# Kernel tuning notes

Measured on AMD Instinct MI355X. Metric: run time of the kernel, lower is better.

## Reference

```python
import jax, jax.numpy as jnp
import numpy as np
from jax import lax

B, N, S, NS, V = 2, 8192, 1024, 32, 8
CF, CIN, COUT, H1, RADIUS = 64, 70, 128, 32, 0.2
BN_EPS = 1e-5


def _bn(x, g, b, axes):
    m = jnp.mean(x, axes, keepdims=True)
    v = jnp.var(x, axes, keepdims=True)
    return (x - m) / jnp.sqrt(v + BN_EPS) * g + b


def _fps(xyz, s):
    # deterministic farthest point sampling, start index 0
    b, n, _ = xyz.shape
    def step(carry, _):
        dmin, last = carry
        p = jnp.take_along_axis(xyz, last[:, None, None], axis=1)[:, 0]  # [B,3]
        d = jnp.sum((xyz - p[:, None, :]) ** 2, -1)
        dmin = jnp.minimum(dmin, d)
        nxt = jnp.argmax(dmin, axis=-1).astype(jnp.int32)
        return (dmin, nxt), last
    init = (jnp.full((b, n), jnp.inf, xyz.dtype), jnp.zeros((b,), jnp.int32))
    _, idx = lax.scan(step, init, None, length=s)
    idx = jnp.transpose(idx)  # [B,S]
    return jnp.take_along_axis(xyz, idx[..., None], axis=1), idx


def _ball_query(new_xyz, xyz, k, radius):
    # first k points (in original order) within radius; -1 padded, like pytorch3d
    b, s, _ = new_xyz.shape
    n = xyz.shape[1]
    d2 = jnp.sum((new_xyz[:, :, None, :] - xyz[:, None, :, :]) ** 2, -1)  # [B,S,N]
    within = d2 < radius * radius
    slot = jnp.cumsum(within.astype(jnp.int32), axis=-1) - 1
    valid = within & (slot < k)
    slot_c = jnp.where(valid, slot, k)  # dump slot k
    bb = jnp.arange(b)[:, None, None]
    ss = jnp.arange(s)[None, :, None]
    upd = jnp.broadcast_to(jnp.arange(n, dtype=jnp.int32), (b, s, n))
    gidx = jnp.full((b, s, k + 1), -1, jnp.int32).at[bb, ss, slot_c].set(upd)[..., :k]
    return gidx


def reference(xyz, f, mc_idx, gumbel_u, W1_0, b1_0, g1_0, be1_0, W1_1, b1_1,
              W2_0, b2_0, g2_0, be2_0, W2_1, b2_1, Wr, br):
    bsz = xyz.shape[0]
    new_xyz, _ = _fps(xyz, S)                              # [B,S,3]
    gidx = _ball_query(new_xyz, xyz, NS, RADIUS)           # [B,S,n]
    mask = gidx < 0
    safe = jnp.where(mask, 0, gidx)
    bb = jnp.arange(bsz)[:, None, None]
    grouped_xyz = jnp.where(mask[..., None], 0.0, xyz[bb, safe])      # [B,S,n,3]
    grouped_feat = jnp.where(mask[..., None], 0.0, f[bb, safe])       # [B,S,n,CF]
    mc = xyz[:, mc_idx, :]                                 # [B,V,3] (same for all S)

    local = grouped_xyz - new_xyz[:, :, None, :]
    gf = jnp.concatenate([grouped_xyz, local, grouped_feat], -1)      # [B,S,n,70]

    arrow = grouped_xyz[:, :, :, None, :] - mc[:, None, None, :, :]   # [B,S,n,V,3]
    eu = jnp.sqrt(jnp.sum(arrow ** 2, -1, keepdims=True))
    gx = jnp.broadcast_to(grouped_xyz[:, :, :, None, :], arrow.shape)
    mcr = jnp.broadcast_to(mc[:, None, None, :, :], arrow.shape)
    rel = jnp.concatenate([-arrow, arrow, eu, gx, mcr], -1)           # [B,S,n,V,13]

    a = jnp.einsum('bsnvi,oi->bsnvo', rel, W1_0) + b1_0
    a = jax.nn.gelu(_bn(a, g1_0, be1_0, (0, 1, 2, 3)), approximate=False)
    a = jnp.einsum('bsnvi,oi->bsnvo', a, W1_1) + b1_1                 # [B,S,n,V,70]

    prod = gf[..., None] * jnp.swapaxes(a, -1, -2)                    # [B,S,n,70,V]
    g = -jnp.log(-jnp.log(gumbel_u))
    soft_w = jax.nn.softmax(prod + g, axis=-1)                        # gumbel softmax, tau=1
    agg = jnp.sum(soft_w * prod, -1)                                  # [B,S,n,70]

    gf2 = jnp.where(mask[..., None], 0.0, agg + gf)

    w = jnp.einsum('bsnc,oc->bsno', gf2, W2_0) + b2_0
    w = jax.nn.gelu(_bn(w, g2_0, be2_0, (0, 1, 2)), approximate=False)
    w = jnp.einsum('bsnc,oc->bsno', w, W2_1) + b2_1                   # [B,S,n,128]

    res = jnp.einsum('bsnc,oc->bsno', gf, Wr) + br
    new_f = jax.nn.gelu(w + res, approximate=False)
    out = jnp.max(new_f, axis=2) + jnp.sum(new_f, axis=2)             # [B,S,128]
    return out, new_xyz


def setup_inputs() -> dict:
    key = jax.random.key(0)
    ks = jax.random.split(key, 18)
    inp = {
        'xyz': jax.random.uniform(ks[0], (B, N, 3), jnp.float32),
        'f': jax.random.normal(ks[1], (B, N, CF), jnp.float32),
        'mc_idx': jax.random.randint(ks[2], (V,), 0, NS),
        'gumbel_u': jax.random.uniform(ks[3], (B, S, NS, CIN, V), jnp.float32, 1e-6, 1.0 - 1e-6),
        'W1_0': jax.random.normal(ks[4], (H1, 13), jnp.float32) / np.sqrt(13.0),
        'b1_0': jnp.zeros((H1,), jnp.float32),
        'g1_0': jnp.ones((H1,), jnp.float32),
        'be1_0': jnp.zeros((H1,), jnp.float32),
        'W1_1': jax.random.normal(ks[5], (CIN, H1), jnp.float32) / np.sqrt(float(H1)),
        'b1_1': jnp.zeros((CIN,), jnp.float32),
        'W2_0': jax.random.normal(ks[6], (COUT, CIN), jnp.float32) / np.sqrt(float(CIN)),
        'b2_0': jnp.zeros((COUT,), jnp.float32),
        'g2_0': jnp.ones((COUT,), jnp.float32),
        'be2_0': jnp.zeros((COUT,), jnp.float32),
        'W2_1': jax.random.normal(ks[7], (COUT, COUT), jnp.float32) / np.sqrt(float(COUT)),
        'b2_1': jnp.zeros((COUT,), jnp.float32),
        'Wr': jax.random.normal(ks[8], (COUT, CIN), jnp.float32) / np.sqrt(float(CIN)),
        'br': jnp.zeros((COUT,), jnp.float32),
    }
    return inp
```

## Files before the change

kernel.cpp:

```cpp
#include <hip/hip_runtime.h>
#include <math.h>

#define NB    2
#define NPTS  8192
#define SSAMP 1024
#define NS    32
#define VV    8
#define CF    64
#define CIN   70
#define COUT  128
#define H1    32

__device__ __forceinline__ float gelu_f(float x){
  return 0.5f*x*(1.0f + erff(x*0.70710678118654752440f));
}

__global__ __launch_bounds__(1024) void k_fps(const float* __restrict__ xyz,
                                              float* __restrict__ new_xyz){
  extern __shared__ unsigned char dynls[];
  float* sx = (float*)dynls;
  float* sy = sx + NPTS;
  float* sz = sy + NPTS;
  unsigned long long* part = (unsigned long long*)(sz + NPTS);

  const int b = blockIdx.x;
  const int t = threadIdx.x;
  const float* X = xyz + (size_t)b * NPTS * 3;
  float px[8], py[8], pz[8], dmin[8];
  unsigned nio[8];
#pragma unroll
  for (int k = 0; k < 8; k++){
    int i = t + k * 1024;
    float x = X[i*3+0], y = X[i*3+1], z = X[i*3+2];
    px[k] = x; py[k] = y; pz[k] = z;
    sx[i] = x; sy[i] = y; sz[i] = z;
    dmin[k] = 3.4e38f;
    nio[k] = ~(unsigned)i;
  }
  __syncthreads();

  int last = 0;
  const int lane = t & 63, wid = t >> 6;
  int pb = 0;
  float* orow = new_xyz + (size_t)b * SSAMP * 3;
  for (int s = 0; s < SSAMP; s++){
    float cx = sx[last], cy = sy[last], cz = sz[last];
    if (t == 0){ orow[0] = cx; orow[1] = cy; orow[2] = cz; orow += 3; }
    unsigned long long bk = 0ull;
#pragma unroll
    for (int k = 0; k < 8; k++){
      float dx = __fsub_rn(px[k], cx);
      float dy = __fsub_rn(py[k], cy);
      float dz = __fsub_rn(pz[k], cz);
      float d  = __fadd_rn(__fadd_rn(__fmul_rn(dx,dx), __fmul_rn(dy,dy)), __fmul_rn(dz,dz));
      d = fminf(dmin[k], d);
      dmin[k] = d;
      unsigned long long key = ((unsigned long long)__float_as_uint(d) << 32) | (unsigned long long)nio[k];
      bk = (key > bk) ? key : bk;
    }
#pragma unroll
    for (int off = 32; off >= 1; off >>= 1){
      unsigned long long o = __shfl_down(bk, off);
      bk = (o > bk) ? o : bk;
    }
    if (lane == 0) part[pb*16 + wid] = bk;
    __syncthreads();
    unsigned long long v[16];
#pragma unroll
    for (int j = 0; j < 16; j++) v[j] = part[pb*16 + j];
#pragma unroll
    for (int st = 8; st >= 1; st >>= 1){
#pragma unroll
      for (int j = 0; j < 8; j++){
        if (j < st) v[j] = (v[j] > v[j+st]) ? v[j] : v[j+st];
      }
    }
    last = (int)(~(unsigned)(v[0] & 0xFFFFFFFFull));
    pb ^= 1;
  }
}

__global__ __launch_bounds__(64) void k_ballq(const float* __restrict__ xyz,
                                              const float* __restrict__ feat,
                                              const float* __restrict__ new_xyz,
                                              float* __restrict__ gf){
  const int bs = blockIdx.x;
  const int b  = bs >> 10;
  const int lane = threadIdx.x;
  const float* X = xyz  + (size_t)b * NPTS * 3;
  const float* F = feat + (size_t)b * NPTS * CF;
  const float cx = new_xyz[bs*3+0], cy = new_xyz[bs*3+1], cz = new_xyz[bs*3+2];
  __shared__ int gid[NS];
  if (lane < NS) gid[lane] = -1;
  __syncthreads();
  const float R2 = (float)(0.2 * 0.2);
  int count = 0;
  for (int base = 0; base < NPTS && count < NS; base += 64){
    int i = base + lane;
    float x = X[i*3+0], y = X[i*3+1], z = X[i*3+2];
    float dx = __fsub_rn(cx,x), dy = __fsub_rn(cy,y), dz = __fsub_rn(cz,z);
    float d2 = __fadd_rn(__fadd_rn(__fmul_rn(dx,dx), __fmul_rn(dy,dy)), __fmul_rn(dz,dz));
    bool within = d2 < R2;
    unsigned long long m = __ballot(within);
    int pre  = __popcll(m & ((1ull << lane) - 1ull));
    int slot = count + pre;
    if (within && slot < NS) gid[slot] = i;
    count += __popcll(m);
  }
  __syncthreads();
  float* grow = gf + (size_t)bs * NS * CIN;
  for (int n = 0; n < NS; n++){
    int gi = gid[n];
    float* row = grow + n * CIN;
    if (gi < 0){
      row[lane] = 0.0f;
      if (lane < CIN - 64) row[64 + lane] = 0.0f;
    } else {
      float gx = X[gi*3+0], gy = X[gi*3+1], gz = X[gi*3+2];
      float v;
      if      (lane == 0) v = gx;
      else if (lane == 1) v = gy;
      else if (lane == 2) v = gz;
      else if (lane == 3) v = __fsub_rn(gx, cx);
      else if (lane == 4) v = __fsub_rn(gy, cy);
      else if (lane == 5) v = __fsub_rn(gz, cz);
      else                v = F[(size_t)gi * CF + (lane - 6)];
      row[lane] = v;
      if (lane < CIN - 64) row[64 + lane] = F[(size_t)gi * CF + 58 + lane];
    }
  }
}

__global__ __launch_bounds__(256) void k_stats1(const float* __restrict__ gf,
                                                const float* __restrict__ xyz,
                                                const int*   __restrict__ mc_idx,
                                                const float* __restrict__ W1_0,
                                                const float* __restrict__ b1_0,
                                                double* __restrict__ stats){
  __shared__ float W10[H1*13];
  __shared__ float b10[H1];
  __shared__ float mcs[NB][VV][3];
  __shared__ float part[4][64];
  const int t = threadIdx.x;
  for (int i = t; i < H1*13; i += 256) W10[i] = W1_0[i];
  if (t < H1) b10[t] = b1_0[t];
  if (t < NB*VV*3){
    int b_ = t / (VV*3), r = t % (VV*3), vv = r / 3, c = r % 3;
    mcs[b_][vv][c] = xyz[(size_t)b_ * NPTS * 3 + (size_t)mc_idx[vv] * 3 + c];
  }
  __syncthreads();
  const int tid = blockIdx.x * 256 + t;
  const int row = tid >> 3, v = tid & 7;
  const int b = row >> 15;
  const float* g = gf + (size_t)row * CIN;
  float gx = g[0], gy = g[1], gz = g[2];
  float mx = mcs[b][v][0], my = mcs[b][v][1], mz = mcs[b][v][2];
  float ax = __fsub_rn(gx,mx), ay = __fsub_rn(gy,my), az = __fsub_rn(gz,mz);
  float eu = sqrtf(__fadd_rn(__fadd_rn(__fmul_rn(ax,ax), __fmul_rn(ay,ay)), __fmul_rn(az,az)));
  float rel[13] = {-ax,-ay,-az, ax,ay,az, eu, gx,gy,gz, mx,my,mz};
  float a1[H1];
#pragma unroll
  for (int h = 0; h < H1; h++){
    float acc = b10[h];
#pragma unroll
    for (int i = 0; i < 13; i++) acc = fmaf(rel[i], W10[h*13+i], acc);
    a1[h] = acc;
  }
  const int lane = t & 63, wid = t >> 6;
  for (int h = 0; h < H1; h++){
    float r1 = a1[h], r2 = a1[h]*a1[h];
#pragma unroll
    for (int off = 32; off >= 1; off >>= 1){
      r1 += __shfl_xor(r1, off);
      r2 += __shfl_xor(r2, off);
    }
    if (lane == 0){ part[wid][h] = r1; part[wid][h+32] = r2; }
  }
  __syncthreads();
  if (t < 64){
    float s = part[0][t] + part[1][t] + part[2][t] + part[3][t];
    atomicAdd(&stats[t], (double)s);
  }
}

__global__ void k_fin1(const double* __restrict__ st, const float* __restrict__ g1,
                       const float* __restrict__ be1, float* __restrict__ AB){
  int t = threadIdx.x;
  if (t < H1){
    double m   = st[t] / 524288.0;
    double var = st[t+32] / 524288.0 - m*m;
    double inv = 1.0 / sqrt(var + 1e-5);
    double A   = (double)g1[t] * inv;
    AB[t]      = (float)A;
    AB[t+H1]   = (float)((double)be1[t] - m*A);
  }
}

__global__ __launch_bounds__(256) void k_mlp1(const float* __restrict__ gf,
                                              const float* __restrict__ gum,
                                              const float* __restrict__ xyz,
                                              const int*   __restrict__ mc_idx,
                                              const float* __restrict__ W1_0,
                                              const float* __restrict__ b1_0,
                                              const float* __restrict__ AB1,
                                              const float* __restrict__ W1_1,
                                              const float* __restrict__ b1_1,
                                              float* __restrict__ gf2){
  __shared__ float W10[H1*13];
  __shared__ float W11[CIN*H1];
  __shared__ float b10[H1], A1s[H1], B1s[H1];
  __shared__ float b11[CIN];
  __shared__ float mcs[NB][VV][3];
  const int t = threadIdx.x;
  for (int i = t; i < H1*13;  i += 256) W10[i] = W1_0[i];
  for (int i = t; i < CIN*H1; i += 256) W11[i] = W1_1[i];
  if (t < H1){ b10[t] = b1_0[t]; A1s[t] = AB1[t]; B1s[t] = AB1[t+H1]; }
  if (t < CIN) b11[t] = b1_1[t];
  if (t < NB*VV*3){
    int b_ = t / (VV*3), r = t % (VV*3), vv = r / 3, c = r % 3;
    mcs[b_][vv][c] = xyz[(size_t)b_ * NPTS * 3 + (size_t)mc_idx[vv] * 3 + c];
  }
  __syncthreads();
  const int tid = blockIdx.x * 256 + t;
  const int row = tid >> 3, v = tid & 7;
  const int b = row >> 15;
  const float* g = gf + (size_t)row * CIN;
  float gx = g[0], gy = g[1], gz = g[2];
  float mx = mcs[b][v][0], my = mcs[b][v][1], mz = mcs[b][v][2];
  float ax = __fsub_rn(gx,mx), ay = __fsub_rn(gy,my), az = __fsub_rn(gz,mz);
  float eu = sqrtf(__fadd_rn(__fadd_rn(__fmul_rn(ax,ax), __fmul_rn(ay,ay)), __fmul_rn(az,az)));
  float rel[13] = {-ax,-ay,-az, ax,ay,az, eu, gx,gy,gz, mx,my,mz};
  float a1g[H1];
#pragma unroll
  for (int h = 0; h < H1; h++){
    float acc = b10[h];
#pragma unroll
    for (int i = 0; i < 13; i++) acc = fmaf(rel[i], W10[h*13+i], acc);
    float x = fmaf(A1s[h], acc, B1s[h]);
    a1g[h] = gelu_f(x);
  }
  const float* gu = gum + (size_t)row * CIN * VV + v;
  for (int c = 0; c < CIN; c++){
    float a2 = b11[c];
#pragma unroll
    for (int h = 0; h < H1; h++) a2 = fmaf(a1g[h], W11[c*H1+h], a2);
    float gfv  = g[c];
    float prod = gfv * a2;
    float u    = gu[c*VV];
    float gg   = -__logf(-__logf(u));
    float tt   = prod + gg;
    float m8   = tt;
#pragma unroll
    for (int m = 1; m < 8; m <<= 1) m8 = fmaxf(m8, __shfl_xor(m8, m));
    float e  = __expf(tt - m8);
    float s1 = e, s2 = e * prod;
#pragma unroll
    for (int m = 1; m < 8; m <<= 1){ s1 += __shfl_xor(s1, m); s2 += __shfl_xor(s2, m); }
    if (v == 0) gf2[(size_t)row * CIN + c] = s2 / s1 + gfv;
  }
}

__global__ __launch_bounds__(256) void k_wpre(const float* __restrict__ gf2,
                                              const float* __restrict__ gf,
                                              const float* __restrict__ W2_0,
                                              const float* __restrict__ b2_0,
                                              const float* __restrict__ Wr,
                                              const float* __restrict__ br,
                                              float* __restrict__ wpre,
                                              float* __restrict__ resb,
                                              double* __restrict__ stats2){
  const int t = threadIdx.x;
  const int c = t & 127, rh = t >> 7;
  float w0[CIN], wr[CIN];
#pragma unroll
  for (int i = 0; i < CIN; i++) w0[i] = W2_0[(size_t)c*CIN + i];
#pragma unroll
  for (int i = 0; i < CIN; i++) wr[i] = Wr[(size_t)c*CIN + i];
  const float bias0 = b2_0[c], biasr = br[c];
  const int base = blockIdx.x * 32;
  float s1 = 0.f, s2 = 0.f;
  for (int j = 0; j < 16; j++){
    int row = base + rh + 2*j;
    const float* g2r = gf2 + (size_t)row * CIN;
    const float* gr  = gf  + (size_t)row * CIN;
    float acc = bias0, accr = biasr;
#pragma unroll
    for (int i = 0; i < CIN; i++){
      float a = g2r[i], b = gr[i];
      acc  = fmaf(a, w0[i], acc);
      accr = fmaf(b, wr[i], accr);
    }
    wpre[(size_t)row*COUT + c] = acc;
    resb[(size_t)row*COUT + c] = accr;
    s1 += acc; s2 += acc*acc;
  }
  __shared__ float buf[256];
  buf[t] = s1; __syncthreads();
  if (t < 128) atomicAdd(&stats2[c], (double)(buf[t] + buf[t+128]));
  __syncthreads();
  buf[t] = s2; __syncthreads();
  if (t < 128) atomicAdd(&stats2[128+c], (double)(buf[t] + buf[t+128]));
}

__global__ void k_fin2(const double* __restrict__ st, const float* __restrict__ g2,
                       const float* __restrict__ be2, float* __restrict__ AB){
  int t = threadIdx.x;
  if (t < COUT){
    double m   = st[t] / 65536.0;
    double var = st[t+128] / 65536.0 - m*m;
    double inv = 1.0 / sqrt(var + 1e-5);
    double A   = (double)g2[t] * inv;
    AB[t]      = (float)A;
    AB[t+COUT] = (float)((double)be2[t] - m*A);
  }
}

__global__ __launch_bounds__(512) void k_final(const float* __restrict__ wpre,
                                               const float* __restrict__ resb,
                                               const float* __restrict__ W2_1,
                                               const float* __restrict__ b2_1,
                                               const float* __restrict__ AB2,
                                               float* __restrict__ out){
  __shared__ float gbuf[4][COUT];
  __shared__ float pm[512], ps[512];
  const int t = threadIdx.x;
  const int o = t & 127, g = t >> 7;
  float w21[COUT];
#pragma unroll
  for (int k = 0; k < COUT; k++) w21[k] = W2_1[(size_t)o*COUT + k];
  const float A2 = AB2[o], B2 = AB2[COUT+o], b21 = b2_1[o];
  const int bs = blockIdx.x * 2 + (g >> 1);
  const int rp = g & 1;
  float vmax = -3.4e38f, vsum = 0.f;
  for (int j = 0; j < 16; j++){
    int n = rp + 2*j;
    int row = bs * NS + n;
    float w  = wpre[(size_t)row*COUT + o];
    float x  = fmaf(A2, w, B2);
    gbuf[g][o] = gelu_f(x);
    __syncthreads();
    float w2 = b21;
#pragma unroll
    for (int k = 0; k < COUT; k++) w2 = fmaf(gbuf[g][k], w21[k], w2);
    float y  = w2 + resb[(size_t)row*COUT + o];
    float nf = gelu_f(y);
    vmax = fmaxf(vmax, nf);
    vsum += nf;
    __syncthreads();
  }
  pm[t] = vmax; ps[t] = vsum;
  __syncthreads();
  if (rp == 0){
    float m = fmaxf(pm[t], pm[t+128]);
    float s = ps[t] + ps[t+128];
    out[(size_t)bs*COUT + o] = m + s;
  }
}

extern "C" void kernel_launch(void* const* d_in, const int* in_sizes, int n_in,
                              void* d_out, int out_size, void* d_ws, size_t ws_size,
                              hipStream_t stream) {
  (void)in_sizes; (void)n_in; (void)out_size; (void)ws_size;
  const float* xyz   = (const float*)d_in[0];
  const float* f     = (const float*)d_in[1];
  const int*   mcid  = (const int*)  d_in[2];
  const float* gum   = (const float*)d_in[3];
  const float* W1_0  = (const float*)d_in[4];
  const float* b1_0  = (const float*)d_in[5];
  const float* g1_0  = (const float*)d_in[6];
  const float* be1_0 = (const float*)d_in[7];
  const float* W1_1  = (const float*)d_in[8];
  const float* b1_1  = (const float*)d_in[9];
  const float* W2_0  = (const float*)d_in[10];
  const float* b2_0  = (const float*)d_in[11];
  const float* g2_0  = (const float*)d_in[12];
  const float* be2_0 = (const float*)d_in[13];
  const float* W2_1  = (const float*)d_in[14];
  const float* b2_1  = (const float*)d_in[15];
  const float* Wr    = (const float*)d_in[16];
  const float* br    = (const float*)d_in[17];

  float* out     = (float*)d_out;
  float* new_xyz = out + (size_t)NB * SSAMP * COUT;

  char*   ws    = (char*)d_ws;
  double* stats = (double*)ws;
  float*  AB1   = (float*)(ws + 2560);
  float*  AB2   = AB1 + 64;
  float*  gfb   = (float*)(ws + 4096);
  const size_t ROWS = (size_t)NB * SSAMP * NS;
  float*  gf2   = gfb + ROWS * CIN;
  float*  wpre  = gf2 + ROWS * CIN;
  float*  resb  = wpre + ROWS * COUT;

  hipMemsetAsync(d_ws, 0, 2560, stream);

  const size_t fps_lds = (size_t)NPTS * 3 * sizeof(float) + 2 * 16 * sizeof(unsigned long long);
  k_fps   <<<NB,              1024, fps_lds, stream>>>(xyz, new_xyz);
  k_ballq <<<NB*SSAMP,        64,   0, stream>>>(xyz, f, new_xyz, gfb);
  k_stats1<<<2048,            256,  0, stream>>>(gfb, xyz, mcid, W1_0, b1_0, stats);
  k_fin1  <<<1,               64,   0, stream>>>(stats, g1_0, be1_0, AB1);
  k_mlp1  <<<2048,            256,  0, stream>>>(gfb, gum, xyz, mcid, W1_0, b1_0, AB1, W1_1, b1_1, gf2);
  k_wpre  <<<2048,            256,  0, stream>>>(gf2, gfb, W2_0, b2_0, Wr, br, wpre, resb, stats + 64);
  k_fin2  <<<1,               128,  0, stream>>>(stats + 64, g2_0, be2_0, AB2);
  k_final <<<1024,            512,  0, stream>>>(wpre, resb, W2_1, b2_1, AB2, out);
}
```

Baseline: 2.182 ms.

## Shrink FPS block to 256 threads with 32 points per thread and cheaper argmax

The farthest-point-sampling kernel now runs 256 threads per batch, each holding 32 points in registers instead of 8, so the cross-wave reduction spans 4 waves instead of 16. The per-thread argmax tracks a float value and a local index rather than building 64-bit keys, and the wave reduction shuffles a float/int pair with a lower-index tie-break. Shared-memory coordinates move to an interleaved xyz layout. This targets the per-iteration barrier and reduction cost of the serial 1024-step loop, at the price of more serial work and higher register pressure per thread.

```diff
diff --git a/kernel.cpp b/kernel.cpp
--- a/kernel.cpp
+++ b/kernel.cpp
@@ -15,27 +15,23 @@
   return 0.5f*x*(1.0f + erff(x*0.70710678118654752440f));
 }
 
-__global__ __launch_bounds__(1024) void k_fps(const float* __restrict__ xyz,
-                                              float* __restrict__ new_xyz){
+__global__ __launch_bounds__(256) void k_fps(const float* __restrict__ xyz,
+                                             float* __restrict__ new_xyz){
   extern __shared__ unsigned char dynls[];
-  float* sx = (float*)dynls;
-  float* sy = sx + NPTS;
-  float* sz = sy + NPTS;
-  unsigned long long* part = (unsigned long long*)(sz + NPTS);
+  float* sxyz = (float*)dynls;
+  unsigned long long* part = (unsigned long long*)(sxyz + NPTS*3);
 
   const int b = blockIdx.x;
   const int t = threadIdx.x;
   const float* X = xyz + (size_t)b * NPTS * 3;
-  float px[8], py[8], pz[8], dmin[8];
-  unsigned nio[8];
-#pragma unroll
-  for (int k = 0; k < 8; k++){
-    int i = t + k * 1024;
+  float px[32], py[32], pz[32], dmin[32];
+#pragma unroll
+  for (int k = 0; k < 32; k++){
+    int i = t + k * 256;
     float x = X[i*3+0], y = X[i*3+1], z = X[i*3+2];
     px[k] = x; py[k] = y; pz[k] = z;
-    sx[i] = x; sy[i] = y; sz[i] = z;
+    sxyz[i*3+0] = x; sxyz[i*3+1] = y; sxyz[i*3+2] = z;
     dmin[k] = 3.4e38f;
-    nio[k] = ~(unsigned)i;
   }
   __syncthreads();
 
@@ -44,38 +40,42 @@
   int pb = 0;
   float* orow = new_xyz + (size_t)b * SSAMP * 3;
   for (int s = 0; s < SSAMP; s++){
-    float cx = sx[last], cy = sy[last], cz = sz[last];
+    float cx = sxyz[last*3+0], cy = sxyz[last*3+1], cz = sxyz[last*3+2];
     if (t == 0){ orow[0] = cx; orow[1] = cy; orow[2] = cz; orow += 3; }
-    unsigned long long bk = 0ull;
-#pragma unroll
-    for (int k = 0; k < 8; k++){
+    float best = -1.0f; int bk = 0;
+#pragma unroll
+    for (int k = 0; k < 32; k++){
       float dx = __fsub_rn(px[k], cx);
       float dy = __fsub_rn(py[k], cy);
       float dz = __fsub_rn(pz[k], cz);
       float d  = __fadd_rn(__fadd_rn(__fmul_rn(dx,dx), __fmul_rn(dy,dy)), __fmul_rn(dz,dz));
       d = fminf(dmin[k], d);
       dmin[k] = d;
-      unsigned long long key = ((unsigned long long)__float_as_uint(d) << 32) | (unsigned long long)nio[k];
-      bk = (key > bk) ? key : bk;
-    }
+      bk   = (d > best) ? k : bk;
+      best = fmaxf(best, d);
+    }
+    int bi = t | (bk << 8);
 #pragma unroll
     for (int off = 32; off >= 1; off >>= 1){
-      unsigned long long o = __shfl_down(bk, off);
-      bk = (o > bk) ? o : bk;
-    }
-    if (lane == 0) part[pb*16 + wid] = bk;
+      float ov = __shfl_down(best, off);
+      int   oi = __shfl_down(bi,   off);
+      bool take = (ov > best) || (ov == best && oi < bi);
+      best = take ? ov : best;
+      bi   = take ? oi : bi;
+    }
+    if (lane == 0){
+      part[pb*4 + wid] = ((unsigned long long)__float_as_uint(best) << 32)
+                       | (unsigned long long)(~(unsigned)bi);
+    }
     __syncthreads();
-    unsigned long long v[16];
-#pragma unroll
-    for (int j = 0; j < 16; j++) v[j] = part[pb*16 + j];
-#pragma unroll
-    for (int st = 8; st >= 1; st >>= 1){
-#pragma unroll
-      for (int j = 0; j < 8; j++){
-        if (j < st) v[j] = (v[j] > v[j+st]) ? v[j] : v[j+st];
-      }
-    }
-    last = (int)(~(unsigned)(v[0] & 0xFFFFFFFFull));
+    unsigned long long v0 = part[pb*4 + 0];
+    unsigned long long v1 = part[pb*4 + 1];
+    unsigned long long v2 = part[pb*4 + 2];
+    unsigned long long v3 = part[pb*4 + 3];
+    unsigned long long m0 = (v0 > v1) ? v0 : v1;
+    unsigned long long m1 = (v2 > v3) ? v2 : v3;
+    unsigned long long m  = (m0 > m1) ? m0 : m1;
+    last = (int)(~(unsigned)(m & 0xFFFFFFFFull));
     pb ^= 1;
   }
 }
@@ -395,8 +395,8 @@
 
   hipMemsetAsync(d_ws, 0, 2560, stream);
 
-  const size_t fps_lds = (size_t)NPTS * 3 * sizeof(float) + 2 * 16 * sizeof(unsigned long long);
-  k_fps   <<<NB,              1024, fps_lds, stream>>>(xyz, new_xyz);
+  const size_t fps_lds = (size_t)NPTS * 3 * sizeof(float) + 2 * 4 * sizeof(unsigned long long);
+  k_fps   <<<NB,              256, fps_lds, stream>>>(xyz, new_xyz);
   k_ballq <<<NB*SSAMP,        64,   0, stream>>>(xyz, f, new_xyz, gfb);
   k_stats1<<<2048,            256,  0, stream>>>(gfb, xyz, mcid, W1_0, b1_0, stats);
   k_fin1  <<<1,               64,   0, stream>>>(stats, g1_0, be1_0, AB1);
```

Measured after the change: 2.049 ms. 1.07x faster.
